# Kernel tuning notes

Hardware: AMD Instinct MI355X
Metric: run time of the kernel (lower is better)

Reference implementation:

```python
import jax, jax.numpy as jnp
import numpy as np

N, E, DIN, GB, GD, LB, LD, G = 50000, 640000, 64, 128, 4, 256, 2, 1024


def setup_inputs() -> dict:
    key = jax.random.key(0)
    ks = jax.random.split(key, 20)
    p = lambda k, shape: (jax.random.normal(k, shape, dtype=jnp.float32) * 0.05)
    return {
        "x": jax.random.normal(ks[0], (N, DIN), dtype=jnp.float32),
        "edge_index": jax.random.randint(ks[1], (2, E), 0, N, dtype=jnp.int64),
        "batch": jnp.sort(jax.random.randint(ks[2], (N,), 0, G, dtype=jnp.int64)),
        "num_graphs": G,
        "W0": p(ks[3], (DIN, GB)), "b0": p(ks[4], (GB,)),
        "Wg": p(ks[5], (GD, GB, GB)), "bg": p(ks[6], (GD, GB)),
        "gamma_g": jnp.ones((GD, GB), jnp.float32), "beta_g": jnp.zeros((GD, GB), jnp.float32),
        "Wl0": p(ks[7], (GB, LB)), "bl0": p(ks[8], (LB,)),
        "Wl": p(ks[9], (LD, LB, LB)), "bl": p(ks[10], (LD, LB)),
        "gamma_l": jnp.ones((LD, LB), jnp.float32), "beta_l": jnp.zeros((LD, LB), jnp.float32),
        "Wout": p(ks[11], (LB, 2)), "bout": p(ks[12], (2,)),
    }


def reference(x, edge_index, batch, num_graphs, W0, b0, Wg, bg, gamma_g, beta_g,
              Wl0, bl0, Wl, bl, gamma_l, beta_l, Wout, bout):
    n = x.shape[0]
    src, dst = edge_index[0], edge_index[1]
    # GCN degree normalization with self loops: deg = 1 + in-degree
    deg = jax.ops.segment_sum(jnp.ones(src.shape[0], x.dtype), dst, num_segments=n) + 1.0
    dinv = jax.lax.rsqrt(deg)                 # deg^{-1/2}
    enorm = dinv[src] * dinv[dst]             # [E] edge norm
    snorm = dinv * dinv                       # [N] self-loop norm (deg^{-1})

    def gcn(h, W, b):
        hw = h @ W                                            # [N, GB]
        agg = jax.ops.segment_sum(hw[src] * enorm[:, None], dst, num_segments=n)
        return agg + hw * snorm[:, None] + b

    def bn(h, g, bt):  # training-mode batchnorm (biased var), eps=1e-5
        m = h.mean(0)
        v = h.var(0)
        return (h - m) * jax.lax.rsqrt(v + 1e-5) * g + bt

    h = jax.nn.relu(gcn(x, W0, b0))
    for i in range(Wg.shape[0]):
        h = jax.nn.relu(bn(gcn(h, Wg[i], bg[i]), gamma_g[i], beta_g[i]))
    # global_add_pool
    hp = jax.ops.segment_sum(h, batch, num_segments=num_graphs)  # [G, GB]
    h = jax.nn.relu(hp @ Wl0 + bl0)
    for i in range(Wl.shape[0]):
        h = jax.nn.relu(bn(h @ Wl[i] + bl[i], gamma_l[i], beta_l[i]))
    return h @ Wout + bout
```

## Files before the change

### kernel.cpp

```cpp
#include <hip/hip_runtime.h>

#define NN 50000
#define EE 640000
#define DINv 64
#define GBv 128
#define GDv 4
#define LBv 256
#define LDv 2
#define GGv 1024

#define NB 196
#define BCAP 4096
#define BTILE 4096
#define NBT ((EE + BTILE - 1) / BTILE)

#define NTILES ((NN + 63) / 64)
#define UPN (NN * 16)
#define CONVN (DINv * GBv + GDv * GBv * GBv)
#define ZEXT 320

typedef _Float16 f16x8 __attribute__((ext_vector_type(8)));
typedef float f32x4 __attribute__((ext_vector_type(4)));

__device__ __forceinline__ float h2f(ushort u) {
  union { ushort u; _Float16 h; } x;
  x.u = u;
  return (float)x.h;
}
__device__ __forceinline__ ushort f2h(float f) {
  union { ushort u; _Float16 h; } x;
  x.h = (_Float16)f;
  return x.u;
}


__global__ __launch_bounds__(256) void k_bucket(const int* __restrict__ ei,
                                                int* __restrict__ bcnt,
                                                uint* __restrict__ bkt) {
  __shared__ int lcnt[NB];
  __shared__ int lbase[NB];
  __shared__ int gbase[NB];
  __shared__ int ls[256];
  __shared__ uint stage[BTILE];
  __shared__ ushort sb[BTILE];
  int tid = threadIdx.x;
  int t0 = blockIdx.x * BTILE;
  int cnt = min(BTILE, EE - t0);
  for (int i = tid; i < NB; i += 256) lcnt[i] = 0;
  __syncthreads();

  uint en[16];
  int bb[16], rk[16];
  int nper = (cnt + 255) >> 8;
  for (int k = 0; k < nper; k++) {
    int e = k * 256 + tid;
    if (e < cnt) {
      int src = ei[t0 + e];
      int dst = ei[EE + t0 + e];
      int b = dst >> 8;
      en[k] = ((uint)src << 8) | (uint)(dst & 255);
      bb[k] = b;
      rk[k] = atomicAdd(&lcnt[b], 1);
    } else {
      bb[k] = -1;
    }
  }
  __syncthreads();

  int v = (tid < NB) ? lcnt[tid] : 0;
  ls[tid] = v;
  __syncthreads();
  for (int off = 1; off < 256; off <<= 1) {
    int t = (tid >= off) ? ls[tid - off] : 0;
    __syncthreads();
    ls[tid] += t;
    __syncthreads();
  }
  if (tid < NB) {
    lbase[tid] = ls[tid] - v;
    gbase[tid] = atomicAdd(&bcnt[tid], v);
  }
  __syncthreads();

  for (int k = 0; k < nper; k++) {
    if (bb[k] >= 0) {
      int slot = lbase[bb[k]] + rk[k];
      stage[slot] = en[k];
      sb[slot] = (ushort)bb[k];
    }
  }
  __syncthreads();

  for (int i = tid; i < cnt; i += 256) {
    int b = sb[i];
    bkt[(size_t)b * BCAP + gbase[b] + (i - lbase[b])] = stage[i];
  }
}


__global__ __launch_bounds__(256) void k_csr(const uint* __restrict__ bkt,
                                             const int* __restrict__ bcnt,
                                             int* __restrict__ offs,
                                             float* __restrict__ dinv,
                                             int* __restrict__ col,
                                             int* __restrict__ deg,
                                             int* __restrict__ ghist) {
  __shared__ int lhist[256];
  __shared__ int lofs[256];
  __shared__ int lcur[256];
  __shared__ int lsb[256];
  __shared__ int lh2[64];
  int b = blockIdx.x;
  int tid = threadIdx.x;
  int bv = (tid < NB) ? bcnt[tid] : 0;
  lsb[tid] = bv;
  lhist[tid] = 0;
  if (tid < 64) lh2[tid] = 0;
  __syncthreads();
  for (int off = 1; off < 256; off <<= 1) {
    int t = (tid >= off) ? lsb[tid - off] : 0;
    __syncthreads();
    lsb[tid] += t;
    __syncthreads();
  }
  int cnt = bcnt[b];
  int rawbase = lsb[b] - cnt;
  int pbase = ((rawbase + 7) & ~7) + b * 2048;
  const uint* B = bkt + (size_t)b * BCAP;
  for (int i = tid; i < cnt; i += 256) atomicAdd(&lhist[B[i] & 255], 1);
  __syncthreads();
  int v = lhist[tid];
  int pv = (v + 7) & ~7;
  lofs[tid] = pv;
  __syncthreads();
  for (int off = 1; off < 256; off <<= 1) {
    int t = (tid >= off) ? lofs[tid - off] : 0;
    __syncthreads();
    lofs[tid] += t;
    __syncthreads();
  }
  int excl = lofs[tid] - pv;
  int n = b * 256 + tid;
  if (n < NN) {
    offs[n] = pbase + excl;
    dinv[n] = rsqrtf((float)(v + 1));
    deg[n] = v;
    atomicAdd(&lh2[min(v, 63)], 1);
    for (int k = v; k < pv; k++) col[pbase + excl + k] = NN;
  }
  lcur[tid] = excl;
  __syncthreads();
  if (tid < 64 && lh2[tid]) atomicAdd(&ghist[tid], lh2[tid]);
  if (b == 0 && tid == 0) dinv[NN] = 0.f;
  for (int i = tid; i < cnt; i += 256) {
    uint e = B[i];
    int p = atomicAdd(&lcur[e & 255], 1);
    col[pbase + p] = (int)(e >> 8);
  }
}


__global__ __launch_bounds__(256) void k_dperm(const int* __restrict__ deg,
                                               const int* __restrict__ ghist,
                                               int* __restrict__ gcur,
                                               int* __restrict__ perm) {
  __shared__ int lhist[64];
  __shared__ int lbase[64];
  int tid = threadIdx.x;
  if (tid < 64) lhist[tid] = 0;
  __syncthreads();
  int n = blockIdx.x * 256 + tid;
  int d = 0, rk = 0;
  if (n < NN) {
    d = min(deg[n], 63);
    rk = atomicAdd(&lhist[d], 1);
  }
  __syncthreads();
  if (tid < 64) {
    int s = 0;
    for (int i = tid + 1; i < 64; i++) s += ghist[i];
    if (lhist[tid]) lbase[tid] = s + atomicAdd(&gcur[tid], lhist[tid]);
  }
  __syncthreads();
  if (n < NN) perm[lbase[d] + rk] = n;
}


__global__ __launch_bounds__(256) void k_prep(const float* __restrict__ x,
                                              const float* __restrict__ dinv,
                                              const float* __restrict__ W0,
                                              const float* __restrict__ Wg,
                                              ushort* __restrict__ u,
                                              ushort* __restrict__ Wt0,
                                              ushort* __restrict__ Wtg,
                                              ushort* __restrict__ g1,
                                              ushort* __restrict__ g2) {
  int idx = blockIdx.x * 256 + threadIdx.x;
  if (idx < UPN) {
    int n = idx >> 4;
    float4 v = ((const float4*)x)[idx];
    float d = dinv[n];
    union { ushort us[4]; uint2 q; } o;
    o.us[0] = f2h(v.x * d);
    o.us[1] = f2h(v.y * d);
    o.us[2] = f2h(v.z * d);
    o.us[3] = f2h(v.w * d);
    ((uint2*)u)[idx] = o.q;
  } else {
    int j = idx - UPN;
    if (j < DINv * GBv) {
      int c = j >> 6, k = j & 63;
      Wt0[j] = f2h(W0[k * GBv + c]);
    } else if (j < CONVN) {
      int e = j - DINv * GBv;
      int i = e >> 14, rem = e & 16383;
      int c = rem >> 7, k = rem & 127;
      Wtg[e] = f2h(Wg[i * GBv * GBv + k * GBv + c]);
    } else if (j < CONVN + ZEXT) {
      int z = j - CONVN;
      if (z < 64) u[(size_t)NN * DINv + z] = 0;
      else if (z < 192) g1[(size_t)NN * GBv + (z - 64)] = 0;
      else g2[(size_t)NN * GBv + (z - 192)] = 0;
    }
  }
}


template <int K, int MODE, bool STATS, bool OUTF>
__global__ __launch_bounds__(512, 2) void k_layer(const ushort* __restrict__ Gin,
                                                  const int* __restrict__ col,
                                                  const int* __restrict__ offs,
                                                  const int* __restrict__ deg,
                                                  const float* __restrict__ dinv,
                                                  const int* __restrict__ perm,
                                                  const float* __restrict__ st,
                                                  const float* __restrict__ gamma,
                                                  const float* __restrict__ beta,
                                                  const ushort* __restrict__ Wt,
                                                  const float* __restrict__ bias,
                                                  float* __restrict__ stG,
                                                  ushort* __restrict__ Gout) {
  constexpr int VEC = K / 16;
  constexpr int KP = K + 8;
  constexpr int CP = 136;
  constexpr bool REUSE = (K == 128);
  __shared__ __attribute__((aligned(16))) _Float16 sW[128 * KP];
  __shared__ __attribute__((aligned(16))) _Float16 sA[64 * KP];
  __shared__ float sB[128];
  __shared__ float ssum[128], ssq[128];
  __shared__ float sDn[64];
  _Float16* sC = REUSE ? sA : sW;
  int tid = threadIdx.x;

  {
    constexpr int CH = K / 8;
    for (int i = tid; i < 128 * CH; i += 512) {
      int c = i / CH, ch = i - c * CH;
      *(uint4*)&sW[c * KP + ch * 8] = ((const uint4*)Wt)[i];
    }
  }
  if (tid < 128) {
    sB[tid] = bias[tid];
    if constexpr (STATS) {
      ssum[tid] = 0.f;
      ssq[tid] = 0.f;
    }
  }

  int w = tid >> 6, lane = tid & 63;
  int quad = lane >> 4, m = lane & 15;
  int row0 = blockIdx.x * 64;

  float sc[VEC], tc[VEC];
  if constexpr (MODE == 2) {
#pragma unroll
    for (int v = 0; v < VEC; v++) {
      int c = m * VEC + v;
      float mu = st[c] * (1.f / NN);
      float var = st[128 + c] * (1.f / NN) - mu * mu;
      float s = rsqrtf(var + 1e-5f) * gamma[c];
      sc[v] = s;
      tc[v] = beta[c] - mu * s;
    }
  }

  union U { uint4 v4; uint2 v2; ushort us[8]; };
  auto loadrow = [&](int s) {
    U u;
    const ushort* p = Gin + (long)s * K + m * VEC;
    if constexpr (VEC == 8) u.v4 = *(const uint4*)p;
    else u.v2 = *(const uint2*)p;
    return u;
  };

  for (int rnd = 0; rnd < 2; rnd++) {
    int r = rnd * 32 + w * 4 + quad;
    int idx = row0 + r;
    float acc[VEC];
#pragma unroll
    for (int v = 0; v < VEC; v++) acc[v] = 0.f;
    float dn = 0.f;
    if (idx < NN) {
      int n = perm[idx];
      dn = dinv[n];
      auto addrow = [&](U u, float wv) {
#pragma unroll
        for (int v = 0; v < VEC; v++) {
          float g = h2f(u.us[v]);
          if constexpr (MODE == 2) g = fmaxf(g * sc[v] + tc[v], 0.f);
          else if constexpr (MODE == 1) g = fmaxf(g, 0.f);
          acc[v] += g * wv;
        }
      };
      addrow(loadrow(n), (MODE == 0) ? 1.f : dn);
      int s0 = offs[n];
      int pcnt = (deg[n] + 7) & ~7;
      const int* cp = col + s0;
      for (int j = 0; j < pcnt; j += 8) {
        int4 ca = *(const int4*)(cp + j);
        int4 cb = *(const int4*)(cp + j + 4);
        int si[8] = {ca.x, ca.y, ca.z, ca.w, cb.x, cb.y, cb.z, cb.w};
        U uu[8];
#pragma unroll
        for (int t = 0; t < 8; t++) uu[t] = loadrow(si[t]);
        float wt[8];
#pragma unroll
        for (int t = 0; t < 8; t++) wt[t] = (MODE == 0) ? 1.f : dinv[si[t]];
#pragma unroll
        for (int t = 0; t < 8; t++) addrow(uu[t], wt[t]);
      }
    }
    if constexpr (OUTF) {
      if (m == 0) sDn[r] = dn;
    }
    U o;
#pragma unroll
    for (int v = 0; v < VEC; v++) o.us[v] = f2h(acc[v] * dn);
    _Float16* ap = &sA[r * KP + m * VEC];
    if constexpr (VEC == 8) *(uint4*)ap = o.v4;
    else *(uint2*)ap = o.v2;
  }
  __syncthreads();

  int wr = w >> 1, wc = w & 1;
  f32x4 acc2[4];
#pragma unroll
  for (int ct = 0; ct < 4; ct++) acc2[ct] = (f32x4){0.f, 0.f, 0.f, 0.f};
  const _Float16* pa = &sA[(16 * wr + m) * KP + quad * 8];
#pragma unroll
  for (int ks = 0; ks < K; ks += 32) {
    f16x8 a = *(const f16x8*)(pa + ks);
#pragma unroll
    for (int ct = 0; ct < 4; ct++) {
      int c = wc * 64 + ct * 16 + m;
      f16x8 bfr = *(const f16x8*)&sW[c * KP + ks + quad * 8];
      acc2[ct] = __builtin_amdgcn_mfma_f32_16x16x32_f16(a, bfr, acc2[ct], 0, 0, 0);
    }
  }

  int crow = 16 * wr + quad * 4;
  float ps[4], pq[4];
  if constexpr (STATS) {
#pragma unroll
    for (int ct = 0; ct < 4; ct++) {
      int c = wc * 64 + ct * 16 + m;
      float bb = sB[c];
      ps[ct] = 0.f;
      pq[ct] = 0.f;
#pragma unroll
      for (int r = 0; r < 4; r++) {
        if (row0 + crow + r < NN) {
          float g = acc2[ct][r] + bb;
          ps[ct] += g;
          pq[ct] += g * g;
        }
      }
    }
  }
  __syncthreads();

  float dvr[4];
  if constexpr (OUTF) {
#pragma unroll
    for (int r = 0; r < 4; r++) dvr[r] = sDn[crow + r];
  }
#pragma unroll
  for (int ct = 0; ct < 4; ct++) {
    int c = wc * 64 + ct * 16 + m;
    float bb = sB[c];
#pragma unroll
    for (int r = 0; r < 4; r++) {
      float y = acc2[ct][r] + bb;
      if constexpr (OUTF) y = fmaxf(y, 0.f) * dvr[r];
      sC[(crow + r) * CP + c] = (_Float16)y;
    }
  }
  __syncthreads();

  {
    int r = tid >> 3;
    int c0 = (tid & 7) * 16;
    int idx2 = row0 + r;
    if (idx2 < NN) {
      int node = perm[idx2];
      const uint4* srcp = (const uint4*)&sC[r * CP + c0];
      uint4* dst = (uint4*)(Gout + (long)node * 128 + c0);
      dst[0] = srcp[0];
      dst[1] = srcp[1];
    }
  }

  if constexpr (STATS) {
#pragma unroll
    for (int ct = 0; ct < 4; ct++) {
      float s = ps[ct], q = pq[ct];
      s += __shfl_xor(s, 16);
      q += __shfl_xor(q, 16);
      s += __shfl_xor(s, 32);
      q += __shfl_xor(q, 32);
      if (quad == 0) {
        atomicAdd(&ssum[wc * 64 + ct * 16 + m], s);
        atomicAdd(&ssq[wc * 64 + ct * 16 + m], q);
      }
    }
    __syncthreads();
    if (tid < 128) {
      int c = (tid + blockIdx.x * 8) & 127;
      atomicAdd(&stG[c], ssum[c]);
      atomicAdd(&stG[128 + c], ssq[c]);
    }
  }
}


__global__ __launch_bounds__(128) void k_pool2(const ushort* __restrict__ G,
                                               const float* __restrict__ st,
                                               const float* __restrict__ gamma,
                                               const float* __restrict__ beta,
                                               const int* __restrict__ batch,
                                               float* __restrict__ hp) {
  __shared__ int sse[2];
  int g = blockIdx.x;
  int c = threadIdx.x;
  if (c < 2) {
    int key = g + c;
    int lo = 0, hi = NN;
    while (lo < hi) {
      int mid = (lo + hi) >> 1;
      if (batch[mid] < key) lo = mid + 1;
      else hi = mid;
    }
    sse[c] = lo;
  }
  __syncthreads();
  int s = sse[0], e = sse[1];
  float m = st[c] * (1.f / NN);
  float v = st[128 + c] * (1.f / NN) - m * m;
  float sc = rsqrtf(v + 1e-5f) * gamma[c];
  float tc = beta[c] - m * sc;
  float a0 = 0.f, a1 = 0.f, a2 = 0.f, a3 = 0.f;
  int n = s;
  for (; n + 3 < e; n += 4) {
    float g0 = h2f(G[(long)(n + 0) * 128 + c]);
    float g1 = h2f(G[(long)(n + 1) * 128 + c]);
    float g2 = h2f(G[(long)(n + 2) * 128 + c]);
    float g3 = h2f(G[(long)(n + 3) * 128 + c]);
    a0 += fmaxf(g0 * sc + tc, 0.f);
    a1 += fmaxf(g1 * sc + tc, 0.f);
    a2 += fmaxf(g2 * sc + tc, 0.f);
    a3 += fmaxf(g3 * sc + tc, 0.f);
  }
  for (; n < e; n++) a0 += fmaxf(h2f(G[(long)n * 128 + c]) * sc + tc, 0.f);
  hp[(long)g * 128 + c] = (a0 + a1) + (a2 + a3);
}


__global__ void k_colstats(const float* __restrict__ X, int rows, float* __restrict__ st) {
  int c = threadIdx.x;
  int C = blockDim.x;
  float s = 0.f, q = 0.f;
  for (int r = blockIdx.x; r < rows; r += gridDim.x) {
    float v = X[(long)r * C + c];
    s += v;
    q += v * v;
  }
  atomicAdd(&st[c], s);
  atomicAdd(&st[C + c], q);
}


template <int KIN, int MODE>
__global__ __launch_bounds__(256) void k_fc(const float* __restrict__ X,
                                            const float* __restrict__ W,
                                            const float* __restrict__ b,
                                            const float* __restrict__ st,
                                            const float* __restrict__ gamma,
                                            const float* __restrict__ beta,
                                            float* __restrict__ Y) {
  __shared__ float sx[KIN];
  int g = blockIdx.x;
  int c = threadIdx.x;
  for (int k = c; k < KIN; k += 256) {
    float v = X[(long)g * KIN + k];
    if constexpr (MODE == 2) {
      float m = st[k] * (1.f / GGv);
      float var = st[KIN + k] * (1.f / GGv) - m * m;
      v = fmaxf((v - m) * rsqrtf(var + 1e-5f) * gamma[k] + beta[k], 0.f);
    }
    sx[k] = v;
  }
  __syncthreads();
  float acc = b[c];
#pragma unroll 8
  for (int k = 0; k < KIN; k++) acc += sx[k] * W[(long)k * 256 + c];
  Y[(long)g * 256 + c] = (MODE == 0) ? fmaxf(acc, 0.f) : acc;
}

__global__ __launch_bounds__(256) void k_out(const float* __restrict__ X,
                                             const float* __restrict__ st,
                                             const float* __restrict__ gamma,
                                             const float* __restrict__ beta,
                                             const float* __restrict__ Wout,
                                             const float* __restrict__ bout,
                                             float* __restrict__ out) {
  int g = blockIdx.x * 4 + (threadIdx.x >> 6);
  int l = threadIdx.x & 63;
  float a0 = 0.f, a1 = 0.f;
  for (int k = l; k < LBv; k += 64) {
    float z = X[(long)g * LBv + k];
    float m = st[k] * (1.f / GGv);
    float var = st[LBv + k] * (1.f / GGv) - m * m;
    float x = fmaxf((z - m) * rsqrtf(var + 1e-5f) * gamma[k] + beta[k], 0.f);
    a0 += x * Wout[2 * k];
    a1 += x * Wout[2 * k + 1];
  }
  for (int off = 32; off > 0; off >>= 1) {
    a0 += __shfl_down(a0, off);
    a1 += __shfl_down(a1, off);
  }
  if (l == 0) {
    out[2 * g] = a0 + bout[0];
    out[2 * g + 1] = a1 + bout[1];
  }
}


extern "C" void kernel_launch(void* const* d_in, const int* in_sizes, int n_in,
                              void* d_out, int out_size, void* d_ws, size_t ws_size,
                              hipStream_t stream) {
  const float* x = (const float*)d_in[0];
  const int* ei = (const int*)d_in[1];
  const int* batch = (const int*)d_in[2];
  const float* W0 = (const float*)d_in[4];
  const float* b0 = (const float*)d_in[5];
  const float* Wg = (const float*)d_in[6];
  const float* bg = (const float*)d_in[7];
  const float* gamma_g = (const float*)d_in[8];
  const float* beta_g = (const float*)d_in[9];
  const float* Wl0 = (const float*)d_in[10];
  const float* bl0 = (const float*)d_in[11];
  const float* Wl = (const float*)d_in[12];
  const float* bl = (const float*)d_in[13];
  const float* gamma_l = (const float*)d_in[14];
  const float* beta_l = (const float*)d_in[15];
  const float* Wout = (const float*)d_in[16];
  const float* bout = (const float*)d_in[17];
  float* out = (float*)d_out;

  char* w = (char*)d_ws;
  auto alloc = [&](size_t bytes) {
    void* p = (void*)w;
    w += (bytes + 255) & ~(size_t)255;
    return p;
  };
  int* bcnt = (int*)alloc((size_t)NB * 4);
  float* stAll = (float*)alloc((size_t)(4 * 256 + 2 * 512) * 4);
  int* ghist = (int*)alloc((size_t)64 * 4);
  int* gcur = (int*)alloc((size_t)64 * 4);
  size_t zspan = (char*)w - (char*)bcnt;
  uint* bkt = (uint*)alloc((size_t)NB * BCAP * 4);
  int* offs = (int*)alloc((size_t)(NN + 1) * 4);
  int* col = (int*)alloc((size_t)(EE + NB * 2048 + 8192) * 4);
  float* dinv = (float*)alloc((size_t)(NN + 1) * 4);
  int* deg = (int*)alloc((size_t)NN * 4);
  int* perm = (int*)alloc((size_t)NN * 4);
  ushort* u = (ushort*)alloc((size_t)(NN + 1) * DINv * 2);
  ushort* g1 = (ushort*)alloc((size_t)(NN + 1) * GBv * 2);
  ushort* g2 = (ushort*)alloc((size_t)(NN + 1) * GBv * 2);
  ushort* Wt0 = (ushort*)alloc((size_t)DINv * GBv * 2);
  ushort* Wtg = (ushort*)alloc((size_t)GDv * GBv * GBv * 2);
  float* hp = (float*)alloc((size_t)GGv * GBv * 4);
  float* m1 = (float*)alloc((size_t)GGv * LBv * 4);
  float* m2 = (float*)alloc((size_t)GGv * LBv * 4);

  float* stg = stAll;
  float* sth0 = stAll + 4 * 256;
  float* sth1 = sth0 + 512;

  hipMemsetAsync(bcnt, 0, zspan, stream);

  k_bucket<<<NBT, 256, 0, stream>>>(ei, bcnt, bkt);
  k_csr<<<NB, 256, 0, stream>>>(bkt, bcnt, offs, dinv, col, deg, ghist);
  k_dperm<<<NB, 256, 0, stream>>>(deg, ghist, gcur, perm);
  k_prep<<<(UPN + CONVN + ZEXT + 255) / 256, 256, 0, stream>>>(x, dinv, W0, Wg, u, Wt0,
                                                               Wtg, g1, g2);

  k_layer<64, 0, false, true><<<NTILES, 512, 0, stream>>>(
      u, col, offs, deg, dinv, perm, nullptr, nullptr, nullptr, Wt0, b0, nullptr, g1);
  k_layer<128, 0, true, false><<<NTILES, 512, 0, stream>>>(
      g1, col, offs, deg, dinv, perm, nullptr, nullptr, nullptr, Wtg, bg, stg, g2);
  for (int i = 1; i < GDv; i++) {
    const ushort* gin = (i & 1) ? g2 : g1;
    ushort* gout = (i & 1) ? g1 : g2;
    k_layer<128, 2, true, false><<<NTILES, 512, 0, stream>>>(
        gin, col, offs, deg, dinv, perm, stg + (size_t)(i - 1) * 256,
        gamma_g + (size_t)(i - 1) * GBv, beta_g + (size_t)(i - 1) * GBv,
        Wtg + (size_t)i * GBv * GBv, bg + (size_t)i * GBv, stg + (size_t)i * 256, gout);
  }

  k_pool2<<<GGv, 128, 0, stream>>>(g1, stg + 3 * 256, gamma_g + 3 * GBv, beta_g + 3 * GBv,
                                   batch, hp);

  k_fc<GBv, 0><<<GGv, 256, 0, stream>>>(hp, Wl0, bl0, nullptr, nullptr, nullptr, m1);
  k_fc<LBv, 1><<<GGv, 256, 0, stream>>>(m1, Wl, bl, nullptr, nullptr, nullptr, m2);
  k_colstats<<<256, LBv, 0, stream>>>(m2, GGv, sth0);
  k_fc<LBv, 2><<<GGv, 256, 0, stream>>>(m2, Wl + (size_t)LBv * LBv, bl + LBv, sth0,
                                        gamma_l, beta_l, m1);
  k_colstats<<<256, LBv, 0, stream>>>(m1, GGv, sth1);
  k_out<<<GGv / 4, 256, 0, stream>>>(m1, sth1, gamma_l + LBv, beta_l + LBv, Wout, bout, out);
}
```

Measured before the change: 409.2 us.

## Double-buffer neighbor row gathers and pad CSR rows to sixteen

Replaces the eight-neighbor gather loop with a software-pipelined loop. Two sets of eight rows are in flight, so the next batch's loads are issued before the current batch is accumulated. CSR row padding grows from 8 to 16 entries, with larger per-bucket slack and a bigger column buffer, so each iteration handles two full batches. The launch-bounds occupancy hint rises from 2 to 3 blocks per CU. The costs are more register pressure from the doubled buffers, and wasted gather work and memory on padding for low-degree nodes.

```diff
diff --git a/kernel.cpp b/kernel.cpp
--- a/kernel.cpp
+++ b/kernel.cpp
@@ -125,12 +125,12 @@
   }
   int cnt = bcnt[b];
   int rawbase = lsb[b] - cnt;
-  int pbase = ((rawbase + 7) & ~7) + b * 2048;
+  int pbase = ((rawbase + 7) & ~7) + b * 4096;
   const uint* B = bkt + (size_t)b * BCAP;
   for (int i = tid; i < cnt; i += 256) atomicAdd(&lhist[B[i] & 255], 1);
   __syncthreads();
   int v = lhist[tid];
-  int pv = (v + 7) & ~7;
+  int pv = (v + 15) & ~15;
   lofs[tid] = pv;
   __syncthreads();
   for (int off = 1; off < 256; off <<= 1) {
@@ -227,7 +227,7 @@
 
 
 template <int K, int MODE, bool STATS, bool OUTF>
-__global__ __launch_bounds__(512, 2) void k_layer(const ushort* __restrict__ Gin,
+__global__ __launch_bounds__(512, 3) void k_layer(const ushort* __restrict__ Gin,
                                                   const int* __restrict__ col,
                                                   const int* __restrict__ offs,
                                                   const int* __restrict__ deg,
@@ -312,22 +312,59 @@
           acc[v] += g * wv;
         }
       };
-      addrow(loadrow(n), (MODE == 0) ? 1.f : dn);
+      auto issue_rows = [&](const int4& c0, const int4& c1, U* uu) {
+        uu[0] = loadrow(c0.x);
+        uu[1] = loadrow(c0.y);
+        uu[2] = loadrow(c0.z);
+        uu[3] = loadrow(c0.w);
+        uu[4] = loadrow(c1.x);
+        uu[5] = loadrow(c1.y);
+        uu[6] = loadrow(c1.z);
+        uu[7] = loadrow(c1.w);
+      };
+      auto consume = [&](const int4& c0, const int4& c1, U* uu) {
+        if constexpr (MODE != 0) {
+          float dd[8];
+          dd[0] = dinv[c0.x];
+          dd[1] = dinv[c0.y];
+          dd[2] = dinv[c0.z];
+          dd[3] = dinv[c0.w];
+          dd[4] = dinv[c1.x];
+          dd[5] = dinv[c1.y];
+          dd[6] = dinv[c1.z];
+          dd[7] = dinv[c1.w];
+#pragma unroll
+          for (int t = 0; t < 8; t++) addrow(uu[t], dd[t]);
+        } else {
+#pragma unroll
+          for (int t = 0; t < 8; t++) addrow(uu[t], 1.f);
+        }
+      };
+
       int s0 = offs[n];
-      int pcnt = (deg[n] + 7) & ~7;
+      int pcnt = (deg[n] + 15) & ~15;
       const int* cp = col + s0;
-      for (int j = 0; j < pcnt; j += 8) {
-        int4 ca = *(const int4*)(cp + j);
-        int4 cb = *(const int4*)(cp + j + 4);
-        int si[8] = {ca.x, ca.y, ca.z, ca.w, cb.x, cb.y, cb.z, cb.w};
-        U uu[8];
-#pragma unroll
-        for (int t = 0; t < 8; t++) uu[t] = loadrow(si[t]);
-        float wt[8];
-#pragma unroll
-        for (int t = 0; t < 8; t++) wt[t] = (MODE == 0) ? 1.f : dinv[si[t]];
-#pragma unroll
-        for (int t = 0; t < 8; t++) addrow(uu[t], wt[t]);
+
+      U uself = loadrow(n);
+      U uA[8], uB[8];
+      int4 a0, a1;
+      if (pcnt > 0) {
+        a0 = *(const int4*)(cp);
+        a1 = *(const int4*)(cp + 4);
+        issue_rows(a0, a1, uA);
+      }
+      addrow(uself, (MODE == 0) ? 1.f : dn);
+      for (int j = 0; j < pcnt; j += 16) {
+        int4 b0 = *(const int4*)(cp + j + 8);
+        int4 b1 = *(const int4*)(cp + j + 12);
+        issue_rows(b0, b1, uB);
+        consume(a0, a1, uA);
+        if (j + 16 < pcnt) {
+          a0 = *(const int4*)(cp + j + 16);
+          a1 = *(const int4*)(cp + j + 20);
+          issue_rows(a0, a1, uA);
+        }
+        consume(b0, b1, uB);
       }
     }
     if constexpr (OUTF) {
@@ -580,7 +617,7 @@
   size_t zspan = (char*)w - (char*)bcnt;
   uint* bkt = (uint*)alloc((size_t)NB * BCAP * 4);
   int* offs = (int*)alloc((size_t)(NN + 1) * 4);
-  int* col = (int*)alloc((size_t)(EE + NB * 2048 + 8192) * 4);
+  int* col = (int*)alloc((size_t)(EE + NB * 4096 + 8192) * 4);
   float* dinv = (float*)alloc((size_t)(NN + 1) * 4);
   int* deg = (int*)alloc((size_t)NN * 4);
   int* perm = (int*)alloc((size_t)NN * 4);
```

After: 545.6 us. +33.3%, slower.
